# Kernel optimization log

Measured on AMD Instinct MI355X. Metric: run time of the kernel, lower is better.

The kernel has to match this reference:

```python
import jax, jax.numpy as jnp
import numpy as np

A_, BS, T, V, E, H, NA = 8, 32, 256, 128, 512, 512, 64

def setup_inputs() -> dict:
    key = jax.random.key(0)
    ks = jax.random.split(key, 6)
    def w(k, shape, fan):
        return (jax.random.normal(k, shape, jnp.float32) / np.sqrt(fan)).astype(jnp.float32)
    return {
        "x": jax.random.normal(ks[0], (A_, BS, T, V), jnp.float32),
        "hidden_states": jnp.zeros((A_, BS, 1, H), jnp.float32),
        "enc_w": w(ks[1], (E, V), V),
        "enc_b": jnp.zeros((E,), jnp.float32),
        "w_ih": w(ks[2], (3 * H, E), E),
        "w_hh": w(ks[3], (3 * H, H), H),
        "b_ih": jnp.zeros((3 * H,), jnp.float32),
        "b_hh": jnp.zeros((3 * H,), jnp.float32),
        "dec_w": w(ks[4], (NA, H), H),
        "dec_b": jnp.zeros((NA,), jnp.float32),
    }

def _gru_scan(enc_t, h0, w_ih, w_hh, b_ih, b_hh):
    # enc_t: [T, N, E], h0: [N, H]. PyTorch GRUCell gate order: r, z, n.
    gi_all = jnp.einsum('tne,ge->tng', enc_t, w_ih) + b_ih  # precompute input projections
    def step(h, gi):
        gh = h @ w_hh.T + b_hh
        i_r, i_z, i_n = jnp.split(gi, 3, axis=-1)
        h_r, h_z, h_n = jnp.split(gh, 3, axis=-1)
        r = jax.nn.sigmoid(i_r + h_r)
        z = jax.nn.sigmoid(i_z + h_z)
        n = jnp.tanh(i_n + r * h_n)
        h_new = (1.0 - z) * n + z * h
        return h_new, h_new
    _, hs = jax.lax.scan(step, h0, gi_all)
    return hs  # [T, N, H]

def reference(x, hidden_states, enc_w, enc_b, w_ih, w_hh, b_ih, b_hh, dec_w, dec_b):
    a, bs, t, v = x.shape
    Hh = hidden_states.shape[-1]
    # MLP encoder: Linear + ReLU over feature dim
    enc = jax.nn.relu(jnp.einsum('abtv,ev->abte', x, enc_w) + enc_b)  # [a,bs,t,E]
    enc_t = enc.reshape(a * bs, t, -1).transpose(1, 0, 2)             # [t, N, E]
    h0 = hidden_states.reshape(a * bs, Hh)
    hs = _gru_scan(enc_t, h0, w_ih, w_hh, b_ih, b_hh)                 # [t, N, H]
    h = hs.transpose(1, 0, 2).reshape(a, bs, t, Hh)                   # [a,bs,t,H]
    f = jax.nn.relu(jnp.einsum('abth,nh->abtn', h, dec_w) + dec_b)    # decoder
    pi = jax.nn.softmax(f, axis=-1)                                   # softmax over v-dim
    return pi, h
```

## Files before the change

### kernel.cpp

```cpp
#include <hip/hip_runtime.h>
#include <hip/hip_bf16.h>

typedef __bf16 bf16x8 __attribute__((ext_vector_type(8)));
typedef float f32x4 __attribute__((ext_vector_type(4)));
typedef unsigned short ushort8 __attribute__((ext_vector_type(8)));
typedef float float4v __attribute__((ext_vector_type(4)));
typedef unsigned long long u64;
typedef unsigned int u32;

#define DEVI __device__ __forceinline__

#define NSEQ 256
#define TT 256
#define VV 128
#define EE 512
#define HH 512
#define NA 64
#define MROWS 65536
#define G3 1536

DEVI unsigned short f2bf(float f) {
  union { float f; unsigned u; } v; v.f = f;
  unsigned r = v.u + 0x7fffu + ((v.u >> 16) & 1u);
  return (unsigned short)(r >> 16);
}
DEVI float bf2f(unsigned short s) {
  union { unsigned u; float f; } v; v.u = ((unsigned)s) << 16;
  return v.f;
}
DEVI bf16x8 ld_bf8_g(const unsigned short* p) {
  ushort8 v = *(const ushort8*)p;
  return __builtin_bit_cast(bf16x8, v);
}
DEVI bf16x8 ld_bf8_b(const char* base, unsigned byte) {
  ushort8 v = *(const ushort8*)(base + byte);
  return __builtin_bit_cast(bf16x8, v);
}
DEVI void gload_lds16(const void* g, unsigned short* lds_base, unsigned lds_byte_off) {
  __builtin_amdgcn_global_load_lds(
      (const __attribute__((address_space(1))) unsigned int*)g,
      (__attribute__((address_space(3))) unsigned int*)(void*)((char*)lds_base + lds_byte_off),
      16, 0, 0);
}

__global__ void cast_f32_bf16(const float* __restrict__ src, unsigned short* __restrict__ dst, int n) {
  int i = blockIdx.x * blockDim.x + threadIdx.x;
  int stride = gridDim.x * blockDim.x;
  for (; i < n; i += stride) dst[i] = f2bf(src[i]);
}

__global__ void zero_u32(u32* __restrict__ p, int n) {
  int i = blockIdx.x * blockDim.x + threadIdx.x;
  if (i < n) p[i] = 0u;
}

template<bool RELU>
__global__ __launch_bounds__(256)
void gemm_bt(const unsigned short* __restrict__ A, const unsigned short* __restrict__ W,
             const float* __restrict__ bias, unsigned short* __restrict__ C,
             int N, int K) {
  __shared__ unsigned short sA[128 * 64];
  __shared__ unsigned short sB[128 * 64];
  const int tid = threadIdx.x;
  const int w = tid >> 6, lane = tid & 63;
  const int l15 = lane & 15, l4 = lane >> 4;
  const int nbn = N >> 7;
  const int bm = blockIdx.x / nbn, bn = blockIdx.x % nbn;

  f32x4 acc[4][4];
  const f32x4 fz = {0.f, 0.f, 0.f, 0.f};
#pragma unroll
  for (int i = 0; i < 4; i++)
#pragma unroll
    for (int j = 0; j < 4; j++) acc[i][j] = fz;

  const int nk = K >> 6;
  for (int bk = 0; bk < nk; ++bk) {
#pragma unroll
    for (int it = 0; it < 4; ++it) {
      int slot = it * 256 + tid;
      int row = slot >> 3, c16 = slot & 7;
      const unsigned short* ga = A + (size_t)(bm * 128 + row) * K + bk * 64 + c16 * 8;
      const unsigned short* gb = W + (size_t)(bn * 128 + row) * K + bk * 64 + c16 * 8;
      unsigned ldsoff = (unsigned)(it * 256 + w * 64) * 16;
      gload_lds16(ga, sA, ldsoff);
      gload_lds16(gb, sB, ldsoff);
    }
    __syncthreads();
#pragma unroll
    for (int kt = 0; kt < 2; ++kt) {
      bf16x8 af[4], bfr[4];
#pragma unroll
      for (int m = 0; m < 4; m++) {
        int row = ((w >> 1) * 64) + m * 16 + l15;
        af[m] = ld_bf8_g(&sA[row * 64 + kt * 32 + l4 * 8]);
      }
#pragma unroll
      for (int n = 0; n < 4; n++) {
        int row = ((w & 1) * 64) + n * 16 + l15;
        bfr[n] = ld_bf8_g(&sB[row * 64 + kt * 32 + l4 * 8]);
      }
#pragma unroll
      for (int m = 0; m < 4; m++)
#pragma unroll
        for (int n = 0; n < 4; n++)
          acc[m][n] = __builtin_amdgcn_mfma_f32_16x16x32_bf16(af[m], bfr[n], acc[m][n], 0, 0, 0);
    }
    __syncthreads();
  }

  const int r0 = bm * 128 + (w >> 1) * 64;
  const int c0 = bn * 128 + (w & 1) * 64;
#pragma unroll
  for (int n = 0; n < 4; n++) {
    int c = c0 + n * 16 + l15;
    float b = bias[c];
#pragma unroll
    for (int m = 0; m < 4; m++)
#pragma unroll
      for (int j = 0; j < 4; j++) {
        int r = r0 + m * 16 + l4 * 4 + j;
        float v = acc[m][n][j] + b;
        if (RELU) v = fmaxf(v, 0.f);
        C[(size_t)r * N + c] = f2bf(v);
      }
  }
}

#define GRU_LDS_BYTES (96 * 1024)

__global__ __launch_bounds__(256, 1)
void gru_scan(const unsigned short* __restrict__ whh,
              const float* __restrict__ b_hh,
              const unsigned short* __restrict__ gi,
              const float* __restrict__ h0f,
              unsigned short* __restrict__ hbA,
              unsigned short* __restrict__ hbB,
              float* __restrict__ hout,
              u32* __restrict__ cnt_base) {
  extern __shared__ char lds[];
  unsigned short* sW = (unsigned short*)lds;

  const int tid = threadIdx.x;
  const int w = tid >> 6, lane = tid & 63, l15 = lane & 15, l4 = lane >> 4;
  const int sg = blockIdx.x >> 4, cg = blockIdx.x & 15;
  const int s0 = sg * 32;
  const int c0 = cg * 32;
  const int mm = w >> 1, e = w & 1;
  u32* cnt = cnt_base + sg * 32;

  for (int it = 0; it < 24; ++it) {
    int slot = it * 256 + tid;
    int lcr = slot >> 6, c16 = slot & 63;
    int grow = (lcr >> 5) * 512 + c0 + (lcr & 31);
    ushort8 v = *(const ushort8*)(whh + (size_t)grow * 512 + c16 * 8);
    unsigned byte = ((unsigned)(lcr * 1024 + c16 * 16)) ^ ((unsigned)(lcr & 7) << 4);
    *(ushort8*)((char*)sW + byte) = v;
  }

  const int c = c0 + e * 16 + l15;
  int rj[4];
#pragma unroll
  for (int j = 0; j < 4; ++j) rj[j] = s0 + mm * 16 + l4 * 4 + j;
  float bias0 = b_hh[c], bias1 = b_hh[512 + c], bias2 = b_hh[1024 + c];
  float hp[4];
#pragma unroll
  for (int j = 0; j < 4; ++j) hp[j] = h0f[(size_t)rj[j] * HH + c];
  size_t houtb[4], gib[4];
#pragma unroll
  for (int j = 0; j < 4; ++j) {
    houtb[j] = (size_t)rj[j] * TT * HH + c;
    gib[j]   = (size_t)rj[j] * TT * G3 + c;
  }
  const int arow = s0 + mm * 16 + l15;
  const unsigned storej = (l15 & 1);

  __syncthreads();

#pragma unroll 1
  for (int t = 0; t < TT; ++t) {
    const unsigned short* rb = (t & 1) ? hbA : hbB;
    unsigned short* wb = (t & 1) ? hbB : hbA;

    float gv0[4], gv1[4], gv2[4];
#pragma unroll
    for (int j = 0; j < 4; ++j) {
      const unsigned short* gp = gi + gib[j] + (size_t)t * G3;
      gv0[j] = bf2f(gp[0]);
      gv1[j] = bf2f(gp[512]);
      gv2[j] = bf2f(gp[1024]);
    }

    if (t > 0) {
      if (tid == 0) {
        unsigned target = 16u * (unsigned)t;
        while (__hip_atomic_load(cnt, __ATOMIC_RELAXED, __HIP_MEMORY_SCOPE_AGENT) < target)
          __builtin_amdgcn_s_sleep(1);
      }
      __syncthreads();
    }

    const unsigned short* ap = rb + (size_t)arow * HH + l4 * 8;
    u64 av[32];
#pragma unroll
    for (int ktg = 0; ktg < 16; ++ktg) {
      av[2 * ktg]     = __hip_atomic_load((const u64*)(ap + ktg * 32),
                                          __ATOMIC_RELAXED, __HIP_MEMORY_SCOPE_AGENT);
      av[2 * ktg + 1] = __hip_atomic_load((const u64*)(ap + ktg * 32 + 4),
                                          __ATOMIC_RELAXED, __HIP_MEMORY_SCOPE_AGENT);
    }

    f32x4 acc[3];
    const f32x4 fz = {0.f, 0.f, 0.f, 0.f};
    acc[0] = fz; acc[1] = fz; acc[2] = fz;
#pragma unroll
    for (int ktg = 0; ktg < 16; ++ktg) {
      union { u64 q[2]; bf16x8 v; } ua;
      ua.q[0] = av[2 * ktg]; ua.q[1] = av[2 * ktg + 1];
      bf16x8 a = ua.v;
#pragma unroll
      for (int g = 0; g < 3; ++g) {
        int lcr = g * 32 + e * 16 + l15;
        unsigned byte = ((unsigned)(lcr * 1024 + ktg * 64 + l4 * 16)) ^ ((unsigned)(lcr & 7) << 4);
        bf16x8 b = ld_bf8_b((const char*)sW, byte);
        acc[g] = __builtin_amdgcn_mfma_f32_16x16x32_bf16(a, b, acc[g], 0, 0, 0);
      }
    }

    float hn[4];
#pragma unroll
    for (int j = 0; j < 4; ++j) {
      float gh0 = acc[0][j] + bias0;
      float gh1 = acc[1][j] + bias1;
      float gh2 = acc[2][j] + bias2;
      float rr = 1.f / (1.f + __expf(-(gv0[j] + gh0)));
      float zz = 1.f / (1.f + __expf(-(gv1[j] + gh1)));
      float nx = gv2[j] + rr * gh2;
      float ex = __expf(2.f * nx);
      float nn = 1.f - 2.f / (ex + 1.f);
      hn[j] = (1.f - zz) * nn + zz * hp[j];
      hp[j] = hn[j];
      hout[houtb[j] + (size_t)t * HH] = hn[j];
    }

#pragma unroll
    for (int j = 0; j < 4; ++j) {
      u32 my = f2bf(hn[j]);
      u32 oth = (u32)__shfl_xor((int)my, 1);
      u32 word = (l15 & 1) ? ((oth & 0xffffu) | (my << 16))
                           : ((my & 0xffffu) | (oth << 16));
      if ((unsigned)(j >> 1) == storej) {
        u32* dst = (u32*)(wb + (size_t)rj[j] * HH + (c & ~1));
        __hip_atomic_store(dst, word, __ATOMIC_RELAXED, __HIP_MEMORY_SCOPE_AGENT);
      }
    }

    __syncthreads();
    if (tid == 0)
      __hip_atomic_fetch_add(cnt, 1u, __ATOMIC_RELAXED, __HIP_MEMORY_SCOPE_AGENT);
  }
}

__global__ __launch_bounds__(256)
void decoder_softmax(const float* __restrict__ hf,
                     const unsigned short* __restrict__ dwb,
                     const float* __restrict__ dec_b,
                     float* __restrict__ pi) {
  __shared__ unsigned short sH[64 * 512];
  const int tid = threadIdx.x, w = tid >> 6, lane = tid & 63, l15 = lane & 15, l4 = lane >> 4;
  const size_t m0 = (size_t)blockIdx.x * 64;

#pragma unroll
  for (int it = 0; it < 16; ++it) {
    int slot = it * 256 + tid;
    int row = slot >> 6, c16 = slot & 63;
    const float* g = hf + (m0 + row) * 512 + c16 * 8;
    float4v v0 = *(const float4v*)g;
    float4v v1 = *(const float4v*)(g + 4);
    ushort8 u;
    u[0] = f2bf(v0[0]); u[1] = f2bf(v0[1]); u[2] = f2bf(v0[2]); u[3] = f2bf(v0[3]);
    u[4] = f2bf(v1[0]); u[5] = f2bf(v1[1]); u[6] = f2bf(v1[2]); u[7] = f2bf(v1[3]);
    unsigned byte = ((unsigned)(row * 1024 + c16 * 16)) ^ ((unsigned)(row & 7) << 4);
    *(ushort8*)((char*)sH + byte) = u;
  }
  __syncthreads();

  f32x4 acc[4];
  const f32x4 fz = {0.f, 0.f, 0.f, 0.f};
#pragma unroll
  for (int n = 0; n < 4; n++) acc[n] = fz;

  for (int kt = 0; kt < 16; ++kt) {
    int row = w * 16 + l15;
    unsigned byte = ((unsigned)(row * 1024 + kt * 64 + l4 * 16)) ^ ((unsigned)(row & 7) << 4);
    bf16x8 a = ld_bf8_b((const char*)sH, byte);
#pragma unroll
    for (int nt = 0; nt < 4; nt++) {
      bf16x8 b = ld_bf8_g(dwb + (size_t)(nt * 16 + l15) * 512 + kt * 32 + l4 * 8);
      acc[nt] = __builtin_amdgcn_mfma_f32_16x16x32_bf16(a, b, acc[nt], 0, 0, 0);
    }
  }

#pragma unroll
  for (int j = 0; j < 4; j++) {
    size_t r = m0 + w * 16 + l4 * 4 + j;
    float v[4];
    float mx = -1e30f;
#pragma unroll
    for (int nt = 0; nt < 4; nt++) {
      v[nt] = fmaxf(acc[nt][j] + dec_b[nt * 16 + l15], 0.f);
      mx = fmaxf(mx, v[nt]);
    }
#pragma unroll
    for (int msk = 1; msk <= 8; msk <<= 1) mx = fmaxf(mx, __shfl_xor(mx, msk));
    float s = 0.f;
#pragma unroll
    for (int nt = 0; nt < 4; nt++) { v[nt] = __expf(v[nt] - mx); s += v[nt]; }
#pragma unroll
    for (int msk = 1; msk <= 8; msk <<= 1) s += __shfl_xor(s, msk);
    float inv = 1.f / s;
#pragma unroll
    for (int nt = 0; nt < 4; nt++) pi[r * 64 + nt * 16 + l15] = v[nt] * inv;
  }
}

extern "C" void kernel_launch(void* const* d_in, const int* in_sizes, int n_in,
                              void* d_out, int out_size, void* d_ws, size_t ws_size,
                              hipStream_t stream) {
  const float* x     = (const float*)d_in[0];
  const float* h0    = (const float*)d_in[1];
  const float* enc_w = (const float*)d_in[2];
  const float* enc_b = (const float*)d_in[3];
  const float* w_ih  = (const float*)d_in[4];
  const float* w_hh  = (const float*)d_in[5];
  const float* b_ih  = (const float*)d_in[6];
  const float* b_hh  = (const float*)d_in[7];
  const float* dec_w = (const float*)d_in[8];
  const float* dec_b = (const float*)d_in[9];

  float* pi_out = (float*)d_out;
  float* h_out  = (float*)d_out + 4194304;

  unsigned short* ws = (unsigned short*)d_ws;
  size_t off = 0;
  unsigned short* x_bf    = ws + off; off += (size_t)MROWS * VV;
  unsigned short* enc_bf  = ws + off; off += (size_t)MROWS * EE;
  unsigned short* gi_bf   = ws + off; off += (size_t)MROWS * G3;
  unsigned short* encw_bf = ws + off; off += (size_t)EE * VV;
  unsigned short* wih_bf  = ws + off; off += (size_t)G3 * EE;
  unsigned short* whh_bf  = ws + off; off += (size_t)G3 * HH;
  unsigned short* decw_bf = ws + off; off += (size_t)NA * HH;
  unsigned short* hb0     = ws + off; off += (size_t)NSEQ * HH;
  unsigned short* hb1     = ws + off; off += (size_t)NSEQ * HH;
  u32*            cnt32   = (u32*)(ws + off); off += 1024;
  (void)ws_size; (void)in_sizes; (void)n_in; (void)out_size;

  hipFuncSetAttribute((const void*)gru_scan,
                      hipFuncAttributeMaxDynamicSharedMemorySize, GRU_LDS_BYTES);

  auto cast = [&](const float* s, unsigned short* d, int n) {
    int blocks = (n + 255) / 256; if (blocks > 2048) blocks = 2048;
    cast_f32_bf16<<<blocks, 256, 0, stream>>>(s, d, n);
  };
  cast(x, x_bf, MROWS * VV);
  cast(enc_w, encw_bf, EE * VV);
  cast(w_ih, wih_bf, G3 * EE);
  cast(w_hh, whh_bf, G3 * HH);
  cast(dec_w, decw_bf, NA * HH);
  cast(h0, hb1, NSEQ * HH);

  zero_u32<<<1, 512, 0, stream>>>(cnt32, 512);

  gemm_bt<true><<<(MROWS / 128) * (EE / 128), 256, 0, stream>>>(x_bf, encw_bf, enc_b, enc_bf, EE, VV);
  gemm_bt<false><<<(MROWS / 128) * (G3 / 128), 256, 0, stream>>>(enc_bf, wih_bf, b_ih, gi_bf, G3, EE);

  gru_scan<<<dim3(128), dim3(256), GRU_LDS_BYTES, stream>>>(
      whh_bf, b_hh, gi_bf, h0, hb0, hb1, h_out, cnt32);

  decoder_softmax<<<1024, 256, 0, stream>>>(h_out, decw_bf, dec_b, pi_out);
}
```

Before: 1.645 ms.

## Replace per-block counter barrier with per-wave flags and wave-level polling in GRU scan

The GRU scan no longer uses one shared counter per sequence group, guarded by __syncthreads and a single polling thread. Each wave now publishes its own step flag and polls only the 32 flags of the waves producing the rows it needs, taking a min-reduction across lanes. The hout float stores move after the flag publish, so they no longer sit on the critical path between steps. This cuts the block-wide barriers and the serialized atomic on every one of the 256 recurrent steps. In exchange it adds more polling traffic, and correctness relies on ordering by vmcnt waits rather than block barriers.

Result: slower. 1.971 ms (+19.8%).

```diff
diff --git a/kernel.cpp b/kernel.cpp
--- a/kernel.cpp
+++ b/kernel.cpp
@@ -137,7 +137,7 @@
               unsigned short* __restrict__ hbA,
               unsigned short* __restrict__ hbB,
               float* __restrict__ hout,
-              u32* __restrict__ cnt_base) {
+              u32* __restrict__ flags) {
   extern __shared__ char lds[];
   unsigned short* sW = (unsigned short*)lds;
 
@@ -147,7 +147,6 @@
   const int s0 = sg * 32;
   const int c0 = cg * 32;
   const int mm = w >> 1, e = w & 1;
-  u32* cnt = cnt_base + sg * 32;
 
   for (int it = 0; it < 24; ++it) {
     int slot = it * 256 + tid;
@@ -175,6 +174,9 @@
   const int arow = s0 + mm * 16 + l15;
   const unsigned storej = (l15 & 1);
 
+  u32* myflag = flags + sg * 128 + mm * 32 + cg * 2 + e;
+  const u32* pollp = flags + sg * 128 + mm * 32 + (lane & 31);
+
   __syncthreads();
 
 #pragma unroll 1
@@ -192,12 +194,16 @@
     }
 
     if (t > 0) {
-      if (tid == 0) {
-        unsigned target = 16u * (unsigned)t;
-        while (__hip_atomic_load(cnt, __ATOMIC_RELAXED, __HIP_MEMORY_SCOPE_AGENT) < target)
-          __builtin_amdgcn_s_sleep(1);
-      }
-      __syncthreads();
+      int mv;
+      do {
+        u32 v = __hip_atomic_load(pollp, __ATOMIC_RELAXED, __HIP_MEMORY_SCOPE_AGENT);
+        mv = (int)v;
+#pragma unroll
+        for (int msk = 1; msk <= 16; msk <<= 1) {
+          int o = __shfl_xor(mv, msk);
+          mv = mv < o ? mv : o;
+        }
+      } while (mv < t);
     }
 
     const unsigned short* ap = rb + (size_t)arow * HH + l4 * 8;
@@ -240,7 +246,6 @@
       float nn = 1.f - 2.f / (ex + 1.f);
       hn[j] = (1.f - zz) * nn + zz * hp[j];
       hp[j] = hn[j];
-      hout[houtb[j] + (size_t)t * HH] = hn[j];
     }
 
 #pragma unroll
@@ -255,9 +260,13 @@
       }
     }
 
-    __syncthreads();
-    if (tid == 0)
-      __hip_atomic_fetch_add(cnt, 1u, __ATOMIC_RELAXED, __HIP_MEMORY_SCOPE_AGENT);
+    asm volatile("s_waitcnt vmcnt(0)" ::: "memory");
+    if (lane == 0)
+      __hip_atomic_store(myflag, (u32)(t + 1), __ATOMIC_RELAXED, __HIP_MEMORY_SCOPE_AGENT);
+
+#pragma unroll
+    for (int j = 0; j < 4; ++j)
+      hout[houtb[j] + (size_t)t * HH] = hn[j];
   }
 }
 
@@ -352,7 +361,7 @@
   unsigned short* decw_bf = ws + off; off += (size_t)NA * HH;
   unsigned short* hb0     = ws + off; off += (size_t)NSEQ * HH;
   unsigned short* hb1     = ws + off; off += (size_t)NSEQ * HH;
-  u32*            cnt32   = (u32*)(ws + off); off += 1024;
+  u32*            flags   = (u32*)(ws + off); off += 2048;
   (void)ws_size; (void)in_sizes; (void)n_in; (void)out_size;
 
   hipFuncSetAttribute((const void*)gru_scan,
@@ -369,13 +378,13 @@
   cast(dec_w, decw_bf, NA * HH);
   cast(h0, hb1, NSEQ * HH);
 
-  zero_u32<<<1, 512, 0, stream>>>(cnt32, 512);
+  zero_u32<<<4, 256, 0, stream>>>(flags, 1024);
 
   gemm_bt<true><<<(MROWS / 128) * (EE / 128), 256, 0, stream>>>(x_bf, encw_bf, enc_b, enc_bf, EE, VV);
   gemm_bt<false><<<(MROWS / 128) * (G3 / 128), 256, 0, stream>>>(enc_bf, wih_bf, b_ih, gi_bf, G3, EE);
 
   gru_scan<<<dim3(128), dim3(256), GRU_LDS_BYTES, stream>>>(
-      whh_bf, b_hh, gi_bf, h0, hb0, hb1, h_out, cnt32);
+      whh_bf, b_hh, gi_bf, h0, hb0, hb1, h_out, flags);
 
   decoder_softmax<<<1024, 256, 0, stream>>>(h_out, decw_bf, dec_b, pi_out);
 }
```
